# Kernel tuning notes

Hardware: AMD Instinct MI355X
Metric: run time of the kernel (lower is better)

## Reference

```python
import jax, jax.numpy as jnp
import numpy as np
import math

B, T, D = 2, 1024, 4096
H, KVH = 32, 8
HD = D // H            # 128
GROUP = H // KVH       # 4
MAX_SEQ = 4096
ROPE_BASE = 10000.0


def rotate_every_two(x):
    # (x0,x1,x2,x3,...) -> (-x1,x0,-x3,x2,...)
    x1 = x[..., ::2]
    x2 = x[..., 1::2]
    return jnp.stack((-x2, x1), axis=-1).reshape(x.shape)


def build_rope_cache():
    inv_freq = 1.0 / (ROPE_BASE ** (jnp.arange(0, HD, 2, dtype=jnp.float32) / HD))
    t = jnp.arange(MAX_SEQ, dtype=jnp.float32)
    freqs = jnp.einsum('i,j->ij', t, inv_freq)        # (MAX_SEQ, HD/2)
    emb = jnp.concatenate([freqs, freqs], axis=-1)    # (MAX_SEQ, HD) -- matches torch cat([freqs,freqs])
    return jnp.cos(emb), jnp.sin(emb)


def setup_inputs() -> dict:
    key = jax.random.key(0)
    kx, kq, kk, kv, ko = jax.random.split(key, 5)
    x = jax.random.normal(kx, (B, T, D), dtype=jnp.float32)
    # weights stored (in_features, out_features)
    wq = jax.random.normal(kq, (D, H * HD), dtype=jnp.float32) * 0.02
    wk = jax.random.normal(kk, (D, KVH * HD), dtype=jnp.float32) * 0.02
    wv = jax.random.normal(kv, (D, KVH * HD), dtype=jnp.float32) * 0.02
    wo = jax.random.normal(ko, (H * HD, D), dtype=jnp.float32) * 0.02
    return {"x": x, "wq": wq, "wk": wk, "wv": wv, "wo": wo, "start_pos": 0}


def reference(x, wq, wk, wv, wo, start_pos):
    cos_cache, sin_cache = build_rope_cache()
    pos = start_pos + jnp.arange(T)
    cos_t = cos_cache[pos][None, None]   # (1,1,T,HD)
    sin_t = sin_cache[pos][None, None]

    q = (x @ wq).reshape(B, T, H, HD).transpose(0, 2, 1, 3)     # (B,H,T,HD)
    k = (x @ wk).reshape(B, T, KVH, HD).transpose(0, 2, 1, 3)   # (B,KVH,T,HD)
    v = (x @ wv).reshape(B, T, KVH, HD).transpose(0, 2, 1, 3)

    q = q * cos_t + rotate_every_two(q) * sin_t
    k = k * cos_t + rotate_every_two(k) * sin_t

    # GQA: repeat-interleave KV heads to match query heads
    k_exp = jnp.repeat(k, GROUP, axis=1)  # (B,H,T,HD)
    v_exp = jnp.repeat(v, GROUP, axis=1)

    scores = jnp.einsum('bhqd,bhkd->bhqk', q, k_exp) / math.sqrt(HD)
    # causal mask (T_q == T_k here): forbid k > q
    mask = jnp.arange(T)[None, :] > jnp.arange(T)[:, None]
    scores = jnp.where(mask[None, None], -jnp.inf, scores)
    attn = jax.nn.softmax(scores, axis=-1)

    out = jnp.einsum('bhqk,bhkd->bhqd', attn, v_exp)
    out = out.transpose(0, 2, 1, 3).reshape(B, T, H * HD)
    return out @ wo
```

## Files before the change

### kernel.cpp

```cpp
#include <hip/hip_runtime.h>
#include <hip/hip_bf16.h>
#include <math.h>

#define B_    2
#define T_    1024
#define D_    4096
#define H_    32
#define KVH_  8
#define HD_   128
#define GROUP_ 4

static constexpr float SCORE_SCALE = 0.08838834764831845f;

typedef __bf16 bf16x8 __attribute__((ext_vector_type(8)));
typedef float  f32x4  __attribute__((ext_vector_type(4)));
typedef unsigned short u16;

__device__ inline float toF(const __hip_bfloat16 v) { return __bfloat162float(v); }
__device__ inline float toF(const float v)          { return v; }

__device__ inline void storeC(float* p, float v)          { *p = v; }
__device__ inline void storeC(__hip_bfloat16* p, float v) { *p = __float2bfloat16(v); }

__device__ inline unsigned short f2bf(float f) {
    union { float f; unsigned u; } v; v.f = f;
    unsigned r = v.u + 0x7FFFu + ((v.u >> 16) & 1u);
    return (unsigned short)(r >> 16);
}

__device__ inline void gload_lds16(const u16* g, u16* l) {
    __builtin_amdgcn_global_load_lds(
        (const __attribute__((address_space(1))) void*)g,
        (__attribute__((address_space(3))) void*)l, 16, 0, 0);
}


__global__ __launch_bounds__(256) void lconv(const float* __restrict__ S,
                                             u16* __restrict__ D, int n8) {
    int i = blockIdx.x * 256 + threadIdx.x;
    if (i >= n8) return;
    const float4 a = *(const float4*)(S + (size_t)i * 8);
    const float4 b = *(const float4*)(S + (size_t)i * 8 + 4);
    union { int4 v; u16 u[8]; } t;
    t.u[0] = f2bf(a.x); t.u[1] = f2bf(a.y); t.u[2] = f2bf(a.z); t.u[3] = f2bf(a.w);
    t.u[4] = f2bf(b.x); t.u[5] = f2bf(b.y); t.u[6] = f2bf(b.z); t.u[7] = f2bf(b.w);
    *(int4*)(D + (size_t)i * 8) = t.v;
}

template <bool DUAL>
__global__ __launch_bounds__(256) void tconv(const float* __restrict__ S0,
                                             u16* __restrict__ D0,
                                             const float* __restrict__ S1,
                                             u16* __restrict__ D1,
                                             int R, int Cc) {
    const float* __restrict__ S = (DUAL && blockIdx.z) ? S1 : S0;
    u16* __restrict__ D         = (DUAL && blockIdx.z) ? D1 : D0;
    __shared__ u16 Tt[64][72];
    const int tid = threadIdx.x;
    const int r0 = blockIdx.y * 64, c0 = blockIdx.x * 64;
    {
        const int rr = tid >> 4, cc4 = (tid & 15) * 4;
#pragma unroll
        for (int e = 0; e < 4; ++e) {
            const int row = rr + e * 16;
            float4 v = *(const float4*)(S + (size_t)(r0 + row) * Cc + c0 + cc4);
            union { int2 w; u16 u[4]; } t;
            t.u[0] = f2bf(v.x); t.u[1] = f2bf(v.y); t.u[2] = f2bf(v.z); t.u[3] = f2bf(v.w);
            *(int2*)&Tt[row][cc4] = t.w;
        }
    }
    __syncthreads();
    {
        const int cc = tid >> 2, r8 = (tid & 3) * 8;
#pragma unroll
        for (int e = 0; e < 2; ++e) {
            const int rb = r8 + e * 32;
            union { int4 v; u16 u[8]; } t;
#pragma unroll
            for (int j = 0; j < 8; ++j) t.u[j] = Tt[rb + j][cc];
            *(int4*)(D + (size_t)(c0 + cc) * R + r0 + rb) = t.v;
        }
    }
}

template <typename TC, bool DUAL, bool TRC1>
__global__ __launch_bounds__(256, 2) void gemm_bf16(const u16* __restrict__ A,
                                                    const u16* __restrict__ Bt0,
                                                    TC* __restrict__ C0,
                                                    const u16* __restrict__ Bt1,
                                                    TC* __restrict__ C1,
                                                    int M, int N, int K) {
    const u16* __restrict__ Bt = (DUAL && blockIdx.z) ? Bt1 : Bt0;
    TC* __restrict__ C         = (DUAL && blockIdx.z) ? C1 : C0;

    __shared__ u16 As[128 * 32];
    __shared__ u16 Bs[128 * 32];

    const int tid   = threadIdx.x;
    const int lane  = tid & 63;
    const int w     = tid >> 6;
    const int waveM = w >> 1;
    const int waveN = w & 1;
    const int lm    = lane & 15;
    const int quad  = lane >> 4;
    const int bm    = blockIdx.y * 128;
    const int bn    = blockIdx.x * 128;

    const int srow = w * 16 + (lane >> 2);
    const int scol = (lane & 3) * 8;

    const u16* agp0 = A  + (size_t)(bm + srow)      * K + scol;
    const u16* agp1 = A  + (size_t)(bm + srow + 64) * K + scol;
    const u16* bgp0 = Bt + (size_t)(bn + srow)      * K + scol;
    const u16* bgp1 = Bt + (size_t)(bn + srow + 64) * K + scol;

    u16* al0 = &As[(w * 16)      * 32];
    u16* al1 = &As[(w * 16 + 64) * 32];
    u16* bl0 = &Bs[(w * 16)      * 32];
    u16* bl1 = &Bs[(w * 16 + 64) * 32];

    f32x4 acc[4][4];
#pragma unroll
    for (int i = 0; i < 4; ++i)
#pragma unroll
        for (int j = 0; j < 4; ++j) acc[i][j] = (f32x4){0.f, 0.f, 0.f, 0.f};

    for (int k0 = 0; k0 < K; k0 += 32) {
        gload_lds16(agp0 + k0, al0);
        gload_lds16(agp1 + k0, al1);
        gload_lds16(bgp0 + k0, bl0);
        gload_lds16(bgp1 + k0, bl1);
        __syncthreads();

        bf16x8 af[4], bfv[4];
#pragma unroll
        for (int i = 0; i < 4; ++i)
            af[i] = *(const bf16x8*)&As[(waveM * 64 + i * 16 + lm) * 32 + quad * 8];
#pragma unroll
        for (int j = 0; j < 4; ++j)
            bfv[j] = *(const bf16x8*)&Bs[(waveN * 64 + j * 16 + lm) * 32 + quad * 8];
#pragma unroll
        for (int i = 0; i < 4; ++i)
#pragma unroll
            for (int j = 0; j < 4; ++j)
                acc[i][j] = __builtin_amdgcn_mfma_f32_16x16x32_bf16(af[i], bfv[j], acc[i][j], 0, 0, 0);
        __syncthreads();
    }

    if (TRC1 && DUAL && blockIdx.z) {
#pragma unroll
        for (int i = 0; i < 4; ++i) {
            int row0 = bm + waveM * 64 + i * 16 + quad * 4;
#pragma unroll
            for (int j = 0; j < 4; ++j) {
                int col = bn + waveN * 64 + j * 16 + lm;
#pragma unroll
                for (int rr = 0; rr < 4; ++rr)
                    storeC(&C[(size_t)col * M + row0 + rr], acc[i][j][rr]);
            }
        }
    } else {
#pragma unroll
        for (int i = 0; i < 4; ++i) {
            int row0 = bm + waveM * 64 + i * 16 + quad * 4;
#pragma unroll
            for (int j = 0; j < 4; ++j) {
                int col = bn + waveN * 64 + j * 16 + lm;
#pragma unroll
                for (int rr = 0; rr < 4; ++rr)
                    storeC(&C[(size_t)(row0 + rr) * N + col], acc[i][j][rr]);
            }
        }
    }
}

#define LSTR 40

template <typename TA, typename TB, typename TC, bool DUAL, bool TRC1>
__global__ __launch_bounds__(256) void gemm_mfma(const TA* __restrict__ A,
                                                 const TB* __restrict__ B0,
                                                 TC* __restrict__ C0,
                                                 const TB* __restrict__ B1,
                                                 TC* __restrict__ C1,
                                                 int M, int N, int K) {
    const TB* __restrict__ B = (DUAL && blockIdx.z) ? B1 : B0;
    TC* __restrict__ C       = (DUAL && blockIdx.z) ? C1 : C0;

    __shared__ unsigned short As[128 * LSTR];
    __shared__ unsigned short Bs[128 * LSTR];

    const int tid   = threadIdx.x;
    const int lane  = tid & 63;
    const int wv    = tid >> 6;
    const int waveM = wv >> 1;
    const int waveN = wv & 1;
    const int lm    = lane & 15;
    const int quad  = lane >> 4;
    const int bm    = blockIdx.y * 128;
    const int bn    = blockIdx.x * 128;

    f32x4 acc[4][4];
#pragma unroll
    for (int i = 0; i < 4; ++i)
#pragma unroll
        for (int j = 0; j < 4; ++j) acc[i][j] = (f32x4){0.f, 0.f, 0.f, 0.f};

    for (int k0 = 0; k0 < K; k0 += 32) {
#pragma unroll
        for (int e = 0; e < 8; ++e) {
            int p  = tid + e * 256;
            int r  = p >> 4, c2 = (p & 15) * 2;
            const TA* ap = A + (size_t)(bm + r) * K + k0 + c2;
            ushort2 t;
            t.x = f2bf(toF(ap[0]));
            t.y = f2bf(toF(ap[1]));
            *(ushort2*)&As[r * LSTR + c2] = t;
        }
#pragma unroll
        for (int e = 0; e < 8; ++e) {
            int p  = tid + e * 256;
            int n  = p & 127, k2 = (p >> 7) * 2;
            const TB* bp = B + (size_t)(k0 + k2) * N + bn + n;
            ushort2 t;
            t.x = f2bf(toF(bp[0]));
            t.y = f2bf(toF(bp[N]));
            *(ushort2*)&Bs[n * LSTR + k2] = t;
        }
        __syncthreads();

        bf16x8 af[4], bfr[4];
#pragma unroll
        for (int i = 0; i < 4; ++i)
            af[i] = *(const bf16x8*)&As[(waveM * 64 + i * 16 + lm) * LSTR + quad * 8];
#pragma unroll
        for (int j = 0; j < 4; ++j)
            bfr[j] = *(const bf16x8*)&Bs[(waveN * 64 + j * 16 + lm) * LSTR + quad * 8];
#pragma unroll
        for (int i = 0; i < 4; ++i)
#pragma unroll
            for (int j = 0; j < 4; ++j)
                acc[i][j] = __builtin_amdgcn_mfma_f32_16x16x32_bf16(af[i], bfr[j], acc[i][j], 0, 0, 0);
        __syncthreads();
    }

    if (TRC1 && DUAL && blockIdx.z) {
#pragma unroll
        for (int i = 0; i < 4; ++i) {
            int row0 = bm + waveM * 64 + i * 16 + quad * 4;
#pragma unroll
            for (int j = 0; j < 4; ++j) {
                int col = bn + waveN * 64 + j * 16 + lm;
#pragma unroll
                for (int rr = 0; rr < 4; ++rr)
                    storeC(&C[(size_t)col * M + row0 + rr], acc[i][j][rr]);
            }
        }
    } else {
#pragma unroll
        for (int i = 0; i < 4; ++i) {
            int row0 = bm + waveM * 64 + i * 16 + quad * 4;
#pragma unroll
            for (int j = 0; j < 4; ++j) {
                int col = bn + waveN * 64 + j * 16 + lm;
#pragma unroll
                for (int rr = 0; rr < 4; ++rr)
                    storeC(&C[(size_t)(row0 + rr) * N + col], acc[i][j][rr]);
            }
        }
    }
}

template <typename TQ, typename TK>
__global__ __launch_bounds__(256) void rope_kernel(TQ* __restrict__ Q,
                                                   TK* __restrict__ Kt,
                                                   const int* __restrict__ start_pos) {
    int w    = blockIdx.x * 4 + (threadIdx.x >> 6);
    int lane = threadIdx.x & 63;
    int hh = w % (H_ + KVH_);
    int n  = w / (H_ + KVH_);
    int t  = n % T_;
    int pos = *start_pos + t;

    int e0 = 2 * lane, e1 = 2 * lane + 1;
    int j0 = e0 & 63,  j1 = e1 & 63;
    const double LN_BASE = 9.210340371976184;
    double a0 = (double)pos * exp(-((double)(2 * j0) / 128.0) * LN_BASE);
    double a1 = (double)pos * exp(-((double)(2 * j1) / 128.0) * LN_BASE);
    float c0 = (float)cos(a0), s0 = (float)sin(a0);
    float c1 = (float)cos(a1), s1 = (float)sin(a1);

    if (hh < H_) {
        TQ* base = Q + (size_t)n * (H_ * HD_) + hh * HD_;
        float x0 = toF(base[e0]), x1 = toF(base[e1]);
        storeC(&base[e0], x0 * c0 - x1 * s0);
        storeC(&base[e1], x1 * c1 + x0 * s1);
    } else {
        TK* base = Kt + (size_t)n * (KVH_ * HD_) + (hh - H_) * HD_;
        float x0 = toF(base[e0]), x1 = toF(base[e1]);
        storeC(&base[e0], x0 * c0 - x1 * s0);
        storeC(&base[e1], x1 * c1 + x0 * s1);
    }
}

#define KSTR 136
#define VSTR 72
#define PSTR 72

__global__ __launch_bounds__(256, 2) void flash_attn(
        const float* __restrict__ Q,
        const __hip_bfloat16* __restrict__ K,
        const __hip_bfloat16* __restrict__ Vt,
        __hip_bfloat16* __restrict__ AO) {
    __shared__ unsigned short Ks[64 * KSTR];
    __shared__ unsigned short Vs[128 * VSTR];
    __shared__ unsigned short Ps[4][16 * PSTR];

    const int tid  = threadIdx.x;
    const int lane = tid & 63;
    const int w    = tid >> 6;
    const int quad = lane >> 4;
    const int lm   = lane & 15;

    const int qt  = (blockIdx.x + blockIdx.y) & 15;
    const int qb  = qt * 64;
    const int h   = blockIdx.y;
    const int b   = blockIdx.z;
    const int kvh = h >> 2;

    const int qw = qb + w * 16;

    bf16x8 qf[4];
    {
        const float* qrow = Q + (size_t)(b * T_ + qw + lm) * (H_ * HD_) + h * HD_;
#pragma unroll
        for (int ks = 0; ks < 4; ++ks) {
            const float* p4 = qrow + ks * 32 + quad * 8;
            float4 f0 = *(const float4*)(p4);
            float4 f1 = *(const float4*)(p4 + 4);
            union { bf16x8 v; unsigned short u[8]; } t;
            t.u[0] = f2bf(f0.x * SCORE_SCALE); t.u[1] = f2bf(f0.y * SCORE_SCALE);
            t.u[2] = f2bf(f0.z * SCORE_SCALE); t.u[3] = f2bf(f0.w * SCORE_SCALE);
            t.u[4] = f2bf(f1.x * SCORE_SCALE); t.u[5] = f2bf(f1.y * SCORE_SCALE);
            t.u[6] = f2bf(f1.z * SCORE_SCALE); t.u[7] = f2bf(f1.w * SCORE_SCALE);
            qf[ks] = t.v;
        }
    }

    float mI[4], lI[4];
    f32x4 o[8];
#pragma unroll
    for (int rr = 0; rr < 4; ++rr) { mI[rr] = -1e30f; lI[rr] = 0.f; }
#pragma unroll
    for (int dc = 0; dc < 8; ++dc) o[dc] = (f32x4){0.f, 0.f, 0.f, 0.f};

    const int nkt = qt + 1;

    for (int kt = 0; kt < nkt; ++kt) {
        const int t0 = kt * 64;
#pragma unroll
        for (int e = 0; e < 4; ++e) {
            int p = tid + e * 256;
            int tt = p >> 4, d0 = (p & 15) * 8;
            int4 v = *(const int4*)(K + (size_t)(b * T_ + t0 + tt) * (KVH_ * HD_) + kvh * HD_ + d0);
            *(int4*)&Ks[tt * KSTR + d0] = v;
        }
#pragma unroll
        for (int e = 0; e < 4; ++e) {
            int p = tid + e * 256;
            int d = p >> 3, tm = (p & 7) * 8;
            int4 v = *(const int4*)(Vt + (size_t)(kvh * HD_ + d) * (B_ * T_) + b * T_ + t0 + tm);
            *(int4*)&Vs[d * VSTR + tm] = v;
        }
        __syncthreads();

        f32x4 s[4];
#pragma unroll
        for (int tc = 0; tc < 4; ++tc) s[tc] = (f32x4){0.f, 0.f, 0.f, 0.f};
        __builtin_amdgcn_s_setprio(1);
#pragma unroll
        for (int ks = 0; ks < 4; ++ks) {
            bf16x8 kf[4];
#pragma unroll
            for (int tc = 0; tc < 4; ++tc)
                kf[tc] = *(const bf16x8*)&Ks[(tc * 16 + lm) * KSTR + ks * 32 + quad * 8];
#pragma unroll
            for (int tc = 0; tc < 4; ++tc)
                s[tc] = __builtin_amdgcn_mfma_f32_16x16x32_bf16(qf[ks], kf[tc], s[tc], 0, 0, 0);
        }
        __builtin_amdgcn_s_setprio(0);

        if (t0 + 63 > qw) {
            int qrow = qw + quad * 4;
#pragma unroll
            for (int tc = 0; tc < 4; ++tc) {
                int tcol = t0 + tc * 16 + lm;
#pragma unroll
                for (int rr = 0; rr < 4; ++rr)
                    if (tcol > qrow + rr) s[tc][rr] = -1e30f;
            }
        }

#pragma unroll
        for (int rr = 0; rr < 4; ++rr) {
            float tmx = fmaxf(fmaxf(s[0][rr], s[1][rr]),
                              fmaxf(s[2][rr], s[3][rr]));
#pragma unroll
            for (int off = 8; off >= 1; off >>= 1)
                tmx = fmaxf(tmx, __shfl_xor(tmx, off, 64));
            float mn    = fmaxf(mI[rr], tmx);
            float alpha = __expf(mI[rr] - mn);
            mI[rr]  = mn;
            float rs = 0.f;
#pragma unroll
            for (int tc = 0; tc < 4; ++tc) {
                float p = __expf(s[tc][rr] - mn);
                s[tc][rr] = p;
                rs += p;
            }
#pragma unroll
            for (int off = 8; off >= 1; off >>= 1)
                rs += __shfl_xor(rs, off, 64);
            lI[rr] = lI[rr] * alpha + rs;
#pragma unroll
            for (int dc = 0; dc < 8; ++dc)
                o[dc][rr] *= alpha;
        }

#pragma unroll
        for (int tc = 0; tc < 4; ++tc)
#pragma unroll
            for (int rr = 0; rr < 4; ++rr)
                Ps[w][(quad * 4 + rr) * PSTR + tc * 16 + lm] = f2bf(s[tc][rr]);

        __builtin_amdgcn_s_setprio(1);
#pragma unroll
        for (int ss = 0; ss < 2; ++ss) {
            bf16x8 pf = *(const bf16x8*)&Ps[w][lm * PSTR + ss * 32 + quad * 8];
#pragma unroll
            for (int dc = 0; dc < 8; ++dc) {
                bf16x8 vf = *(const bf16x8*)&Vs[(dc * 16 + lm) * VSTR + ss * 32 + quad * 8];
                o[dc] = __builtin_amdgcn_mfma_f32_16x16x32_bf16(pf, vf, o[dc], 0, 0, 0);
            }
        }
        __builtin_amdgcn_s_setprio(0);
        __syncthreads();
    }

#pragma unroll
    for (int rr = 0; rr < 4; ++rr) {
        float inv = 1.f / lI[rr];
        size_t row = (size_t)(b * T_ + qw + quad * 4 + rr) * (H_ * HD_) + h * HD_;
#pragma unroll
        for (int dc = 0; dc < 8; ++dc)
            AO[row + dc * 16 + lm] = __float2bfloat16(o[dc][rr] * inv);
    }
}

extern "C" void kernel_launch(void* const* d_in, const int* in_sizes, int n_in,
                              void* d_out, int out_size, void* d_ws, size_t ws_size,
                              hipStream_t stream) {
    const float* x  = (const float*)d_in[0];
    const float* wq = (const float*)d_in[1];
    const float* wk = (const float*)d_in[2];
    const float* wv = (const float*)d_in[3];
    const float* wo = (const float*)d_in[4];
    const int* start_pos = (const int*)d_in[5];
    float* out = (float*)d_out;

    dim3 blk(256);
    const int M   = B_ * T_;
    const int NQ  = H_ * HD_;
    const int NKV = KVH_ * HD_;

    const size_t NEED = 58720256;

    if (ws_size >= NEED) {
        char* w = (char*)d_ws;
        __hip_bfloat16* Kb  = (__hip_bfloat16*)(w);
        __hip_bfloat16* Vtb = (__hip_bfloat16*)(w + (4u  << 20));
        u16*            xb  = (u16*)(w + (8u  << 20));
        __hip_bfloat16* AOb = (__hip_bfloat16*)(w + (8u  << 20));
        u16*            wS  = (u16*)(w + (24u << 20));
        u16* wqb = wS;
        u16* wkb = wS;
        u16* wvb = wS + (size_t)NKV * D_;
        u16* wob = wS;
        float* Qf = out;

        lconv<<<(M * D_ / 8 + 255) / 256, blk, 0, stream>>>(x, xb, M * D_ / 8);
        tconv<false><<<dim3(NQ / 64, D_ / 64, 1), blk, 0, stream>>>(wq, wqb, nullptr, nullptr, D_, NQ);
        gemm_bf16<float, false, false>
            <<<dim3(NQ / 128, M / 128, 1), blk, 0, stream>>>(xb, wqb, Qf, nullptr, nullptr, M, NQ, D_);
        tconv<true><<<dim3(NKV / 64, D_ / 64, 2), blk, 0, stream>>>(wk, wkb, wv, wvb, D_, NKV);
        gemm_bf16<__hip_bfloat16, true, true>
            <<<dim3(NKV / 128, M / 128, 2), blk, 0, stream>>>(xb, wkb, Kb, wvb, Vtb, M, NKV, D_);
        rope_kernel<<<(M * (H_ + KVH_)) / 4, blk, 0, stream>>>(Qf, Kb, start_pos);
        tconv<false><<<dim3(NQ / 64, NQ / 64, 1), blk, 0, stream>>>(wo, wob, nullptr, nullptr, NQ, D_);
        flash_attn<<<dim3(T_ / 64, H_, B_), blk, 0, stream>>>(Qf, Kb, Vtb, AOb);
        gemm_bf16<float, false, false>
            <<<dim3(D_ / 128, M / 128, 1), blk, 0, stream>>>((const u16*)AOb, wob, out, nullptr, nullptr, M, D_, NQ);
    } else {
        float* Qf           = out;
        __hip_bfloat16* Kb  = (__hip_bfloat16*)d_ws;
        __hip_bfloat16* Vtb = Kb + (size_t)B_ * T_ * KVH_ * HD_;
        __hip_bfloat16* AOb = Vtb + (size_t)B_ * T_ * KVH_ * HD_;

        gemm_mfma<float, float, float, false, false>
            <<<dim3(NQ / 128, M / 128, 1), blk, 0, stream>>>(x, wq, Qf, nullptr, nullptr, M, NQ, D_);
        gemm_mfma<float, float, __hip_bfloat16, true, true>
            <<<dim3(NKV / 128, M / 128, 2), blk, 0, stream>>>(x, wk, Kb, wv, Vtb, M, NKV, D_);
        rope_kernel<<<(M * (H_ + KVH_)) / 4, blk, 0, stream>>>(Qf, Kb, start_pos);
        flash_attn<<<dim3(T_ / 64, H_, B_), blk, 0, stream>>>(Qf, Kb, Vtb, AOb);
        gemm_mfma<__hip_bfloat16, float, float, false, false>
            <<<dim3(D_ / 128, M / 128, 1), blk, 0, stream>>>(AOb, wo, out, nullptr, nullptr, M, D_, NQ);
    }
}
```

Baseline: 589.7 us.

## Store Q in bf16, vectorize per-token RoPE, apply score scale after QK

The Q projection GEMM now writes bf16 instead of fp32 into the output buffer. This halves Q traffic through the GEMM store, the RoPE pass and the flash-attention Q load. A new per-token RoPE kernel computes cos/sin once per token in shared memory using float math, then rotates Q and K with 16-byte vector loads and stores, replacing the per-element double-precision trig kernel. The softmax scale moves from the Q conversion to the fp32 scores after the QK MFMA. This adds an extra bf16 rounding of Q before RoPE, and the RoPE angles are computed in float rather than double, both of which may shift accuracy.

New measurement: 547.5 us. 1.08x faster.

```diff
diff --git a/kernel.cpp b/kernel.cpp
--- a/kernel.cpp
+++ b/kernel.cpp
@@ -26,6 +26,10 @@
     union { float f; unsigned u; } v; v.f = f;
     unsigned r = v.u + 0x7FFFu + ((v.u >> 16) & 1u);
     return (unsigned short)(r >> 16);
+}
+
+__device__ inline float bf2f(u16 u) {
+    union { float f; unsigned u; } v; v.u = (unsigned)u << 16; return v.f;
 }
 
 __device__ inline void gload_lds16(const u16* g, u16* l) {
@@ -270,6 +274,53 @@
     }
 }
 
+__device__ inline void rope_apply8(__hip_bfloat16* p, const float* cs,
+                                   const float* sn, int t0) {
+    union { int4 v; u16 u[8]; } in, outv;
+    in.v = *(const int4*)p;
+    float x[8];
+#pragma unroll
+    for (int i = 0; i < 8; ++i) x[i] = bf2f(in.u[i]);
+#pragma unroll
+    for (int pr = 0; pr < 4; ++pr) {
+        float c0 = cs[t0 + 2 * pr],     s0 = sn[t0 + 2 * pr];
+        float c1 = cs[t0 + 2 * pr + 1], s1 = sn[t0 + 2 * pr + 1];
+        float e = x[2 * pr], o = x[2 * pr + 1];
+        outv.u[2 * pr]     = f2bf(e * c0 - o * s0);
+        outv.u[2 * pr + 1] = f2bf(o * c1 + e * s1);
+    }
+    *(int4*)p = outv.v;
+}
+
+__global__ __launch_bounds__(256) void rope_tok(__hip_bfloat16* __restrict__ Q,
+                                                __hip_bfloat16* __restrict__ K,
+                                                const int* __restrict__ start_pos) {
+    __shared__ float cs[64], sn[64];
+    const int n   = blockIdx.x;
+    const int tid = threadIdx.x;
+    const int pos = *start_pos + (n % T_);
+
+    if (tid < 64) {
+        float invf = exp2f(-(float)tid * 0.20762050593045232f);
+        float ang  = (float)pos * invf;
+        float s, c;
+        __sincosf(ang, &s, &c);
+        s = sinf(ang); c = cosf(ang);
+        cs[tid] = c; sn[tid] = s;
+    }
+    __syncthreads();
+
+    __hip_bfloat16* qrow = Q + (size_t)n * (H_ * HD_);
+    __hip_bfloat16* krow = K + (size_t)n * (KVH_ * HD_);
+#pragma unroll
+    for (int e = 0; e < 2; ++e) {
+        int g = tid + e * 256;
+        rope_apply8(qrow + g * 8, cs, sn, (g * 8) & 63);
+    }
+    if (tid < 128)
+        rope_apply8(krow + tid * 8, cs, sn, (tid * 8) & 63);
+}
+
 template <typename TQ, typename TK>
 __global__ __launch_bounds__(256) void rope_kernel(TQ* __restrict__ Q,
                                                    TK* __restrict__ Kt,
@@ -306,8 +357,9 @@
 #define VSTR 72
 #define PSTR 72
 
+template <typename TQ>
 __global__ __launch_bounds__(256, 2) void flash_attn(
-        const float* __restrict__ Q,
+        const TQ* __restrict__ Q,
         const __hip_bfloat16* __restrict__ K,
         const __hip_bfloat16* __restrict__ Vt,
         __hip_bfloat16* __restrict__ AO) {
@@ -331,18 +383,24 @@
 
     bf16x8 qf[4];
     {
-        const float* qrow = Q + (size_t)(b * T_ + qw + lm) * (H_ * HD_) + h * HD_;
-#pragma unroll
-        for (int ks = 0; ks < 4; ++ks) {
-            const float* p4 = qrow + ks * 32 + quad * 8;
-            float4 f0 = *(const float4*)(p4);
-            float4 f1 = *(const float4*)(p4 + 4);
-            union { bf16x8 v; unsigned short u[8]; } t;
-            t.u[0] = f2bf(f0.x * SCORE_SCALE); t.u[1] = f2bf(f0.y * SCORE_SCALE);
-            t.u[2] = f2bf(f0.z * SCORE_SCALE); t.u[3] = f2bf(f0.w * SCORE_SCALE);
-            t.u[4] = f2bf(f1.x * SCORE_SCALE); t.u[5] = f2bf(f1.y * SCORE_SCALE);
-            t.u[6] = f2bf(f1.z * SCORE_SCALE); t.u[7] = f2bf(f1.w * SCORE_SCALE);
-            qf[ks] = t.v;
+        const TQ* qrow = Q + (size_t)(b * T_ + qw + lm) * (H_ * HD_) + h * HD_;
+        if constexpr (sizeof(TQ) == 2) {
+#pragma unroll
+            for (int ks = 0; ks < 4; ++ks)
+                qf[ks] = *(const bf16x8*)(qrow + ks * 32 + quad * 8);
+        } else {
+#pragma unroll
+            for (int ks = 0; ks < 4; ++ks) {
+                const TQ* p4 = qrow + ks * 32 + quad * 8;
+                float4 f0 = *(const float4*)(p4);
+                float4 f1 = *(const float4*)(p4 + 4);
+                union { bf16x8 v; unsigned short u[8]; } t;
+                t.u[0] = f2bf(toF(f0.x)); t.u[1] = f2bf(toF(f0.y));
+                t.u[2] = f2bf(toF(f0.z)); t.u[3] = f2bf(toF(f0.w));
+                t.u[4] = f2bf(toF(f1.x)); t.u[5] = f2bf(toF(f1.y));
+                t.u[6] = f2bf(toF(f1.z)); t.u[7] = f2bf(toF(f1.w));
+                qf[ks] = t.v;
+            }
         }
     }
 
@@ -388,6 +446,11 @@
                 s[tc] = __builtin_amdgcn_mfma_f32_16x16x32_bf16(qf[ks], kf[tc], s[tc], 0, 0, 0);
         }
         __builtin_amdgcn_s_setprio(0);
+
+#pragma unroll
+        for (int tc = 0; tc < 4; ++tc)
+#pragma unroll
+            for (int rr = 0; rr < 4; ++rr) s[tc][rr] *= SCORE_SCALE;
 
         if (t0 + 63 > qw) {
             int qrow = qw + quad * 4;
@@ -485,18 +548,18 @@
         u16* wkb = wS;
         u16* wvb = wS + (size_t)NKV * D_;
         u16* wob = wS;
-        float* Qf = out;
+        __hip_bfloat16* Qb = (__hip_bfloat16*)d_out;
 
         lconv<<<(M * D_ / 8 + 255) / 256, blk, 0, stream>>>(x, xb, M * D_ / 8);
         tconv<false><<<dim3(NQ / 64, D_ / 64, 1), blk, 0, stream>>>(wq, wqb, nullptr, nullptr, D_, NQ);
-        gemm_bf16<float, false, false>
-            <<<dim3(NQ / 128, M / 128, 1), blk, 0, stream>>>(xb, wqb, Qf, nullptr, nullptr, M, NQ, D_);
+        gemm_bf16<__hip_bfloat16, false, false>
+            <<<dim3(NQ / 128, M / 128, 1), blk, 0, stream>>>(xb, wqb, Qb, nullptr, nullptr, M, NQ, D_);
         tconv<true><<<dim3(NKV / 64, D_ / 64, 2), blk, 0, stream>>>(wk, wkb, wv, wvb, D_, NKV);
         gemm_bf16<__hip_bfloat16, true, true>
             <<<dim3(NKV / 128, M / 128, 2), blk, 0, stream>>>(xb, wkb, Kb, wvb, Vtb, M, NKV, D_);
-        rope_kernel<<<(M * (H_ + KVH_)) / 4, blk, 0, stream>>>(Qf, Kb, start_pos);
+        rope_tok<<<M, blk, 0, stream>>>(Qb, Kb, start_pos);
         tconv<false><<<dim3(NQ / 64, NQ / 64, 1), blk, 0, stream>>>(wo, wob, nullptr, nullptr, NQ, D_);
-        flash_attn<<<dim3(T_ / 64, H_, B_), blk, 0, stream>>>(Qf, Kb, Vtb, AOb);
+        flash_attn<__hip_bfloat16><<<dim3(T_ / 64, H_, B_), blk, 0, stream>>>(Qb, Kb, Vtb, AOb);
         gemm_bf16<float, false, false>
             <<<dim3(D_ / 128, M / 128, 1), blk, 0, stream>>>((const u16*)AOb, wob, out, nullptr, nullptr, M, D_, NQ);
     } else {
@@ -510,7 +573,7 @@
         gemm_mfma<float, float, __hip_bfloat16, true, true>
             <<<dim3(NKV / 128, M / 128, 2), blk, 0, stream>>>(x, wk, Kb, wv, Vtb, M, NKV, D_);
         rope_kernel<<<(M * (H_ + KVH_)) / 4, blk, 0, stream>>>(Qf, Kb, start_pos);
-        flash_attn<<<dim3(T_ / 64, H_, B_), blk, 0, stream>>>(Qf, Kb, Vtb, AOb);
+        flash_attn<float><<<dim3(T_ / 64, H_, B_), blk, 0, stream>>>(Qf, Kb, Vtb, AOb);
         gemm_mfma<__hip_bfloat16, float, float, false, false>
             <<<dim3(D_ / 128, M / 128, 1), blk, 0, stream>>>(AOb, wo, out, nullptr, nullptr, M, D_, NQ);
     }
```
